# Kernel optimization log

Hardware: AMD Instinct MI355X
Metric: run time of the kernel (lower is better)

Reference implementation:

```python
import jax, jax.numpy as jnp
import numpy as np

B, S, D, H = 2, 2048, 1024, 16
MASK_VAL = -50000.0

def setup_inputs() -> dict:
    key = jax.random.key(0)
    k1, k2, k3, k4 = jax.random.split(key, 4)
    # weights stored as [in, out] so projection is x @ W (equals torch Linear with W.T)
    s = 1.0 / np.sqrt(D)
    return {
        "x": jax.random.normal(k1, (B, S, D), dtype=jnp.float32),
        "Wq": jax.random.normal(k2, (D, D), dtype=jnp.float32) * s,
        "Wkv": jax.random.normal(k3, (D, 2 * D), dtype=jnp.float32) * s,
        "Wo": jax.random.normal(k4, (D, D), dtype=jnp.float32) * s,
    }

def reference(x, Wq, Wkv, Wo):
    b, sl, d = x.shape
    h = H
    hd = d // h
    scale = hd ** (-0.5)
    q = x @ Wq                      # [b, sl, d]
    kv = x @ Wkv                    # [b, sl, 2d]
    k, v = jnp.split(kv, 2, axis=-1)
    # [b, h, s, hd]
    q = q.reshape(b, sl, h, hd).transpose(0, 2, 1, 3)
    k = k.reshape(b, sl, h, hd).transpose(0, 2, 1, 3)
    v = v.reshape(b, sl, h, hd).transpose(0, 2, 1, 3)
    dots = jnp.einsum('bhid,bhjd->bhij', q * scale, k)  # [b,h,s,s]
    # causal: strictly-upper-triangular entries set to MASK_VAL
    causal = jnp.tril(jnp.ones((sl, sl), dtype=bool))
    dots = jnp.where(causal, dots, MASK_VAL)
    attn = jax.nn.softmax(dots, axis=-1)
    out = jnp.einsum('bhij,bhjd->bihd', attn, v).reshape(b, sl, d)
    return out @ Wo
```

## Files before the change

kernel.cpp:

```cpp
#include <hip/hip_runtime.h>

typedef __bf16 bf16_t;
typedef unsigned short u16;
typedef __attribute__((ext_vector_type(8))) __bf16 bf16x8;
typedef __attribute__((ext_vector_type(4))) float f32x4;
typedef __attribute__((ext_vector_type(4))) u16 u16x4;
typedef __attribute__((ext_vector_type(8))) u16 u16x8;

#define SS 2048
#define PSTR 72

__device__ __forceinline__ u16 f2b(float f) {
    return __builtin_bit_cast(u16, (__bf16)f);
}

__device__ __forceinline__ float fexp2(float x) {
#if __has_builtin(__builtin_amdgcn_exp2f)
    return __builtin_amdgcn_exp2f(x);
#else
    float r;
    asm("v_exp_f32 %0, %1" : "=v"(r) : "v"(x));
    return r;
#endif
}

__device__ __forceinline__ void async_copy16(const u16* g, u16* l) {
    __builtin_amdgcn_global_load_lds(
        (__attribute__((address_space(1))) void*)(u16*)g,
        (__attribute__((address_space(3))) void*)l, 16, 0, 0);
}

__device__ __forceinline__ bf16x8 ldfrag(const u16* p) {
    return __builtin_bit_cast(bf16x8, *(const u16x8*)p);
}

__global__ __launch_bounds__(256)
void cast_x_kernel(const float* __restrict__ x, u16* __restrict__ xb) {
    size_t i = ((size_t)blockIdx.x * 256 + threadIdx.x) * 8;
    float4 a = *(const float4*)(x + i);
    float4 b = *(const float4*)(x + i + 4);
    u16x8 o;
    o[0] = f2b(a.x); o[1] = f2b(a.y); o[2] = f2b(a.z); o[3] = f2b(a.w);
    o[4] = f2b(b.x); o[5] = f2b(b.y); o[6] = f2b(b.z); o[7] = f2b(b.w);
    *(u16x8*)(xb + i) = o;
}

__global__ __launch_bounds__(256)
void transpose_all(const float* __restrict__ Wq, const float* __restrict__ Wkv,
                   const float* __restrict__ Wo, u16* __restrict__ WcatT,
                   u16* __restrict__ WoT) {
    const int z = blockIdx.z;
    if (z != 1 && blockIdx.y >= 16) return;
    const float* src; u16* dst; int N; float scale;
    if (z == 0)      { src = Wq;  dst = WcatT;               N = 1024; scale = 0.125f * 1.44269504089f; }
    else if (z == 1) { src = Wkv; dst = WcatT + 1024 * 1024; N = 2048; scale = 1.0f; }
    else             { src = Wo;  dst = WoT;                 N = 1024; scale = 1.0f; }
    __shared__ __attribute__((aligned(16))) u16 tile[64][72];
    const int k0 = blockIdx.x * 64, n0 = blockIdx.y * 64;
    const int tid = threadIdx.x;
#pragma unroll
    for (int p = 0; p < 4; ++p) {
        int c = p * 256 + tid;
        int r = c >> 4, c4 = c & 15;
        float4 v = *(const float4*)(src + (size_t)(k0 + r) * N + n0 + c4 * 4);
        u16x4 o;
        o[0] = f2b(v.x * scale); o[1] = f2b(v.y * scale);
        o[2] = f2b(v.z * scale); o[3] = f2b(v.w * scale);
        *(u16x4*)&tile[r][c4 * 4] = o;
    }
    __syncthreads();
#pragma unroll
    for (int p = 0; p < 4; ++p) {
        int c = p * 256 + tid;
        int n = c >> 4, k4 = c & 15;
        u16x4 o;
#pragma unroll
        for (int i = 0; i < 4; ++i) o[i] = tile[k4 * 4 + i][n];
        *(u16x4*)(dst + (size_t)(n0 + n) * 1024 + k0 + k4 * 4) = o;
    }
}

__global__ __launch_bounds__(256)
void transpose_v(const u16* __restrict__ QKV, u16* __restrict__ VTg) {
    __shared__ __attribute__((aligned(16))) u16 tile[64][72];
    const int s0 = blockIdx.x * 64;
    const int bh = blockIdx.y;
    const int b = bh >> 4, h = bh & 15;
    const int tid = threadIdx.x;
    const u16* src = QKV + ((size_t)b * SS + s0) * 3072 + 2048 + h * 64;
#pragma unroll
    for (int p = 0; p < 4; ++p) {
        int c = p * 256 + tid;
        int s = c >> 4, h4 = c & 15;
        *(u16x4*)&tile[s][h4 * 4] = *(const u16x4*)(src + (size_t)s * 3072 + h4 * 4);
    }
    __syncthreads();
    u16* dst = VTg + (size_t)bh * 64 * 2048 + s0;
#pragma unroll
    for (int p = 0; p < 4; ++p) {
        int c = p * 256 + tid;
        int hd = c >> 4, s4 = c & 15;
        u16x4 o;
#pragma unroll
        for (int i = 0; i < 4; ++i) o[i] = tile[s4 * 4 + i][hd];
        *(u16x4*)(dst + (size_t)hd * 2048 + s4 * 4) = o;
    }
}

template <typename OutT>
__global__ __launch_bounds__(256, 2)
void gemm_bt(const u16* __restrict__ A, const u16* __restrict__ BT,
             OutT* __restrict__ C, int M, int N, int K) {
    __shared__ __attribute__((aligned(16))) u16 As[128 * 32];
    __shared__ __attribute__((aligned(16))) u16 Bs[128 * 32];
    const int tid = threadIdx.x;
    const int wave = tid >> 6, lane = tid & 63;
    const int l15 = lane & 15, quad = lane >> 4;
    const int m0 = blockIdx.y * 128, n0 = blockIdx.x * 128;
    const int wm = (wave >> 1) * 64, wn = (wave & 1) * 64;
    const f32x4 zero = {0.f, 0.f, 0.f, 0.f};
    f32x4 acc[4][4];
#pragma unroll
    for (int i = 0; i < 4; ++i)
#pragma unroll
        for (int j = 0; j < 4; ++j) acc[i][j] = zero;
    const int r0 = tid >> 2, kc = (tid & 3) * 8;
    for (int k0 = 0; k0 < K; k0 += 32) {
        async_copy16(A + (size_t)(m0 + r0) * K + k0 + kc, As + tid * 8);
        async_copy16(BT + (size_t)(n0 + r0) * K + k0 + kc, Bs + tid * 8);
        async_copy16(A + (size_t)(m0 + 64 + r0) * K + k0 + kc, As + (256 + tid) * 8);
        async_copy16(BT + (size_t)(n0 + 64 + r0) * K + k0 + kc, Bs + (256 + tid) * 8);
        __syncthreads();
        bf16x8 af[4], bf[4];
#pragma unroll
        for (int t = 0; t < 4; ++t) {
            af[t] = ldfrag(As + (wm + t * 16 + l15) * 32 + quad * 8);
            bf[t] = ldfrag(Bs + (wn + t * 16 + l15) * 32 + quad * 8);
        }
#pragma unroll
        for (int mt = 0; mt < 4; ++mt)
#pragma unroll
            for (int nt = 0; nt < 4; ++nt)
                acc[mt][nt] = __builtin_amdgcn_mfma_f32_16x16x32_bf16(
                    af[mt], bf[nt], acc[mt][nt], 0, 0, 0);
        __syncthreads();
    }
#pragma unroll
    for (int mt = 0; mt < 4; ++mt)
#pragma unroll
        for (int nt = 0; nt < 4; ++nt) {
            const int n = n0 + wn + nt * 16 + l15;
#pragma unroll
            for (int r = 0; r < 4; ++r) {
                const int m = m0 + wm + mt * 16 + quad * 4 + r;
                float v = acc[mt][nt][r];
                if constexpr (sizeof(OutT) == 2) C[(size_t)m * N + n] = (OutT)f2b(v);
                else                             C[(size_t)m * N + n] = v;
            }
        }
}

__global__ __launch_bounds__(256, 2)
void gemm_bt64(const u16* __restrict__ A, const u16* __restrict__ BT,
               float* __restrict__ C, int M, int N, int K) {
    __shared__ __attribute__((aligned(16))) u16 As[128 * 32];
    __shared__ __attribute__((aligned(16))) u16 Bs[64 * 32];
    const int tid = threadIdx.x;
    const int wave = tid >> 6, lane = tid & 63;
    const int l15 = lane & 15, quad = lane >> 4;
    const int m0 = blockIdx.y * 128, n0 = blockIdx.x * 64;
    const int wm = (wave >> 1) * 64, wn = (wave & 1) * 32;
    const f32x4 zero = {0.f, 0.f, 0.f, 0.f};
    f32x4 acc[4][2];
#pragma unroll
    for (int i = 0; i < 4; ++i)
#pragma unroll
        for (int j = 0; j < 2; ++j) acc[i][j] = zero;
    const int r0 = tid >> 2, kc = (tid & 3) * 8;
    for (int k0 = 0; k0 < K; k0 += 32) {
        async_copy16(A + (size_t)(m0 + r0) * K + k0 + kc, As + tid * 8);
        async_copy16(A + (size_t)(m0 + 64 + r0) * K + k0 + kc, As + (256 + tid) * 8);
        async_copy16(BT + (size_t)(n0 + r0) * K + k0 + kc, Bs + tid * 8);
        __syncthreads();
        bf16x8 af[4], bf[2];
#pragma unroll
        for (int t = 0; t < 4; ++t)
            af[t] = ldfrag(As + (wm + t * 16 + l15) * 32 + quad * 8);
#pragma unroll
        for (int t = 0; t < 2; ++t)
            bf[t] = ldfrag(Bs + (wn + t * 16 + l15) * 32 + quad * 8);
#pragma unroll
        for (int mt = 0; mt < 4; ++mt)
#pragma unroll
            for (int nt = 0; nt < 2; ++nt)
                acc[mt][nt] = __builtin_amdgcn_mfma_f32_16x16x32_bf16(
                    af[mt], bf[nt], acc[mt][nt], 0, 0, 0);
        __syncthreads();
    }
#pragma unroll
    for (int mt = 0; mt < 4; ++mt)
#pragma unroll
        for (int nt = 0; nt < 2; ++nt) {
            const int n = n0 + wn + nt * 16 + l15;
#pragma unroll
            for (int r = 0; r < 4; ++r) {
                const int m = m0 + wm + mt * 16 + quad * 4 + r;
                C[(size_t)m * N + n] = acc[mt][nt][r];
            }
        }
}

__device__ __forceinline__ void attn_scoreT(
    const bf16x8 (&kf)[2], const bf16x8 (&qf)[4][2],
    float (&l_i)[4], u16* __restrict__ P, bool diag, int w16, int l15, int quad) {
    const f32x4 cinit = {-10.f, -10.f, -10.f, -10.f};
#pragma unroll
    for (int t = 0; t < 4; ++t) {
        f32x4 a = __builtin_amdgcn_mfma_f32_16x16x32_bf16(kf[0], qf[t][0], cinit, 0, 0, 0);
        f32x4 s = __builtin_amdgcn_mfma_f32_16x16x32_bf16(kf[1], qf[t][1], a, 0, 0, 0);
        if (diag) {
#pragma unroll
            for (int r = 0; r < 4; ++r)
                if (w16 + quad * 4 + r > t * 16 + l15) s[r] = -1e30f;
        }
        u16x4 pk;
        float acc = 0.f;
#pragma unroll
        for (int r = 0; r < 4; ++r) {
            float pv = fexp2(s[r]);
            acc += pv;
            pk[r] = f2b(pv);
        }
        l_i[t] += acc;
        *(u16x4*)(P + (t * 16 + l15) * PSTR + w16 + quad * 4) = pk;
    }
}

__device__ __forceinline__ void attn_pv(
    const u16* __restrict__ P, const bf16x8 (&vf)[4][2],
    f32x4 (&O)[4], int l15, int quad) {
    bf16x8 pf0 = ldfrag(P + l15 * PSTR + quad * 8);
    bf16x8 pf1 = ldfrag(P + l15 * PSTR + 32 + quad * 8);
#pragma unroll
    for (int nt = 0; nt < 4; ++nt) {
        O[nt] = __builtin_amdgcn_mfma_f32_16x16x32_bf16(pf0, vf[nt][0], O[nt], 0, 0, 0);
        O[nt] = __builtin_amdgcn_mfma_f32_16x16x32_bf16(pf1, vf[nt][1], O[nt], 0, 0, 0);
    }
}

__global__ __launch_bounds__(256, 2)
void attn_kernel(const u16* __restrict__ QKV, const u16* __restrict__ VTg,
                 u16* __restrict__ AO) {
    __shared__ __attribute__((aligned(16))) u16 Kt[2][2 * 64 * 32];
    __shared__ __attribute__((aligned(16))) u16 Vt[2][2 * 64 * 32];
    __shared__ __attribute__((aligned(16))) u16 Pq[128 * PSTR];
    const int tid = threadIdx.x;
    const int wave = tid >> 6, lane = tid & 63;
    const int l15 = lane & 15, quad = lane >> 4;
    const int w16 = wave * 16;
    const int bh = blockIdx.y, b = bh >> 4, h = bh & 15;
    const int xe = b ? 15 - (int)blockIdx.x : (int)blockIdx.x;
    const int qbA = 31 - xe, qbB = xe;
    const int qA0 = qbA * 64, qB0 = qbB * 64;
    const size_t bS = (size_t)b * SS;
    const u16* vbase = VTg + (size_t)bh * 64 * 2048;
    const int rr = (tid >> 2) & 63, kc8 = (tid & 3) * 8;

    {
        const u16* qsrcA = QKV + (bS + qA0 + rr) * 3072 + h * 64 + kc8;
        async_copy16(qsrcA,      Pq + tid * 8);
        async_copy16(qsrcA + 32, Pq + (256 + tid) * 8);
        const u16* qsrcB = QKV + (bS + qB0 + rr) * 3072 + h * 64 + kc8;
        async_copy16(qsrcB,      Pq + (512 + tid) * 8);
        async_copy16(qsrcB + 32, Pq + (768 + tid) * 8);
        const u16* ksrc = QKV + (bS + rr) * 3072 + 1024 + h * 64 + kc8;
        async_copy16(ksrc,      Kt[0] + tid * 8);
        async_copy16(ksrc + 32, Kt[0] + (256 + tid) * 8);
        const u16* vsrc = vbase + (size_t)rr * 2048 + kc8;
        async_copy16(vsrc,      Vt[0] + tid * 8);
        async_copy16(vsrc + 32, Vt[0] + (256 + tid) * 8);
    }
    __syncthreads();
    bf16x8 qfA[4][2], qfB[4][2];
#pragma unroll
    for (int t = 0; t < 4; ++t)
#pragma unroll
        for (int ks = 0; ks < 2; ++ks) {
            qfA[t][ks] = ldfrag(Pq + ks * 2048 + (t * 16 + l15) * 32 + quad * 8);
            qfB[t][ks] = ldfrag(Pq + 4096 + ks * 2048 + (t * 16 + l15) * 32 + quad * 8);
        }
    __syncthreads();

    u16* PA = Pq;
    u16* PB = Pq + 64 * PSTR;
    float lA[4], lB[4];
    f32x4 OA[4], OB[4];
    const f32x4 zero = {0.f, 0.f, 0.f, 0.f};
#pragma unroll
    for (int t = 0; t < 4; ++t) { lA[t] = lB[t] = 0.f; }
#pragma unroll
    for (int nt = 0; nt < 4; ++nt) { OA[nt] = zero; OB[nt] = zero; }

    for (int j = 0; j <= qbA; ++j) {
        if (j < qbA) {
            const int kv1 = (j + 1) * 64;
            const int nb = (j + 1) & 1;
            const u16* ksrc = QKV + (bS + kv1 + rr) * 3072 + 1024 + h * 64 + kc8;
            async_copy16(ksrc,      Kt[nb] + tid * 8);
            async_copy16(ksrc + 32, Kt[nb] + (256 + tid) * 8);
            const u16* vsrc = vbase + (size_t)rr * 2048 + kv1 + kc8;
            async_copy16(vsrc,      Vt[nb] + tid * 8);
            async_copy16(vsrc + 32, Vt[nb] + (256 + tid) * 8);
        }
        const bool bAct = (j <= qbB);
        const u16* KB = Kt[j & 1];
        const u16* VB = Vt[j & 1];
        bf16x8 kf[2];
#pragma unroll
        for (int ks = 0; ks < 2; ++ks)
            kf[ks] = ldfrag(KB + ks * 2048 + (w16 + l15) * 32 + quad * 8);
        attn_scoreT(kf, qfA, lA, PA, j == qbA, w16, l15, quad);
        if (bAct)
            attn_scoreT(kf, qfB, lB, PB, j == qbB, w16, l15, quad);
        __syncthreads();
        bf16x8 vf[4][2];
#pragma unroll
        for (int nt = 0; nt < 4; ++nt)
#pragma unroll
            for (int ks = 0; ks < 2; ++ks)
                vf[nt][ks] = ldfrag(VB + ks * 2048 + (nt * 16 + l15) * 32 + quad * 8);
        attn_pv(PA + w16 * PSTR, vf, OA, l15, quad);
        if (bAct)
            attn_pv(PB + w16 * PSTR, vf, OB, l15, quad);
        __syncthreads();
    }

    float* lsh = (float*)Kt;
#pragma unroll
    for (int t = 0; t < 4; ++t) {
        float sA = lA[t];
        sA += __shfl_xor(sA, 16); sA += __shfl_xor(sA, 32);
        float sB = lB[t];
        sB += __shfl_xor(sB, 16); sB += __shfl_xor(sB, 32);
        if (lane < 16) {
            lsh[(t * 16 + l15) * 4 + wave] = sA;
            lsh[(64 + t * 16 + l15) * 4 + wave] = sB;
        }
    }
    __syncthreads();
#pragma unroll
    for (int r = 0; r < 4; ++r) {
        const int qlA = w16 + quad * 4 + r;
        f32x4 la = *(const f32x4*)&lsh[qlA * 4];
        f32x4 lb = *(const f32x4*)&lsh[(64 + qlA) * 4];
        float invA = 1.0f / (la[0] + la[1] + la[2] + la[3]);
        float invB = 1.0f / (lb[0] + lb[1] + lb[2] + lb[3]);
        size_t rowA = bS + (size_t)qA0 + qlA;
        size_t rowB = bS + (size_t)qB0 + qlA;
#pragma unroll
        for (int nt = 0; nt < 4; ++nt) {
            AO[rowA * 1024 + h * 64 + nt * 16 + l15] = f2b(OA[nt][r] * invA);
            AO[rowB * 1024 + h * 64 + nt * 16 + l15] = f2b(OB[nt][r] * invB);
        }
    }
}

extern "C" void kernel_launch(void* const* d_in, const int* in_sizes, int n_in,
                              void* d_out, int out_size, void* d_ws, size_t ws_size,
                              hipStream_t stream) {
    (void)in_sizes; (void)n_in; (void)out_size; (void)ws_size;
    const float* x   = (const float*)d_in[0];
    const float* Wq  = (const float*)d_in[1];
    const float* Wkv = (const float*)d_in[2];
    const float* Wo  = (const float*)d_in[3];
    float* out = (float*)d_out;
    char* ws = (char*)d_ws;
    u16* xb    = (u16*)(ws);
    u16* WcatT = (u16*)(ws + (size_t)(8 << 20));
    u16* WoT   = (u16*)(ws + (size_t)(14 << 20));
    u16* QKV   = (u16*)(ws + (size_t)(16 << 20));
    u16* VTb   = (u16*)(ws + (size_t)(40 << 20));
    u16* AO    = xb;

    cast_x_kernel<<<2048, 256, 0, stream>>>(x, xb);
    transpose_all<<<dim3(16, 32, 3), 256, 0, stream>>>(Wq, Wkv, Wo, WcatT, WoT);
    gemm_bt<u16><<<dim3(24, 32), 256, 0, stream>>>(xb, WcatT, QKV, 4096, 3072, 1024);
    transpose_v<<<dim3(32, 32), 256, 0, stream>>>(QKV, VTb);
    attn_kernel<<<dim3(16, 32), 256, 0, stream>>>(QKV, VTb, AO);
    gemm_bt64<<<dim3(16, 32), 256, 0, stream>>>(AO, WoT, out, 4096, 1024, 1024);
}
```

Baseline: 183.5 us.

## Load K and V fragments directly from global into registers, drop LDS staging

Removes the shared-memory double buffers for K and V tiles and instead has each wave load its K fragment (software-prefetched one iteration ahead into a register double buffer) and all V fragments directly from global memory. The intent is to cut LDS traffic, async-copy overhead and LDS footprint, which could allow more occupancy. In exchange, every wave redundantly fetches the full V tile from global/L2 each iteration, V loads are no longer prefetched ahead, and the reduction scratch moves onto the P buffer.

```diff
diff --git a/kernel.cpp b/kernel.cpp
--- a/kernel.cpp
+++ b/kernel.cpp
@@ -251,8 +251,6 @@
 __global__ __launch_bounds__(256, 2)
 void attn_kernel(const u16* __restrict__ QKV, const u16* __restrict__ VTg,
                  u16* __restrict__ AO) {
-    __shared__ __attribute__((aligned(16))) u16 Kt[2][2 * 64 * 32];
-    __shared__ __attribute__((aligned(16))) u16 Vt[2][2 * 64 * 32];
     __shared__ __attribute__((aligned(16))) u16 Pq[128 * PSTR];
     const int tid = threadIdx.x;
     const int wave = tid >> 6, lane = tid & 63;
@@ -264,6 +262,7 @@
     const int qA0 = qbA * 64, qB0 = qbB * 64;
     const size_t bS = (size_t)b * SS;
     const u16* vbase = VTg + (size_t)bh * 64 * 2048;
+    const u16* kbase = QKV + bS * 3072 + 1024 + h * 64;
     const int rr = (tid >> 2) & 63, kc8 = (tid & 3) * 8;
 
     {
@@ -273,12 +272,6 @@
         const u16* qsrcB = QKV + (bS + qB0 + rr) * 3072 + h * 64 + kc8;
         async_copy16(qsrcB,      Pq + (512 + tid) * 8);
         async_copy16(qsrcB + 32, Pq + (768 + tid) * 8);
-        const u16* ksrc = QKV + (bS + rr) * 3072 + 1024 + h * 64 + kc8;
-        async_copy16(ksrc,      Kt[0] + tid * 8);
-        async_copy16(ksrc + 32, Kt[0] + (256 + tid) * 8);
-        const u16* vsrc = vbase + (size_t)rr * 2048 + kc8;
-        async_copy16(vsrc,      Vt[0] + tid * 8);
-        async_copy16(vsrc + 32, Vt[0] + (256 + tid) * 8);
     }
     __syncthreads();
     bf16x8 qfA[4][2], qfB[4][2];
@@ -301,41 +294,42 @@
 #pragma unroll
     for (int nt = 0; nt < 4; ++nt) { OA[nt] = zero; OB[nt] = zero; }
 
+    bf16x8 kf[2][2];
+    {
+        const u16* kp = kbase + (size_t)(w16 + l15) * 3072 + quad * 8;
+        kf[0][0] = ldfrag(kp);
+        kf[0][1] = ldfrag(kp + 32);
+    }
+
     for (int j = 0; j <= qbA; ++j) {
+        const int kv0 = j * 64;
+        bf16x8 vf[4][2];
+        {
+            const u16* vp = vbase + (size_t)l15 * 2048 + kv0 + quad * 8;
+#pragma unroll
+            for (int nt = 0; nt < 4; ++nt)
+#pragma unroll
+                for (int ks = 0; ks < 2; ++ks)
+                    vf[nt][ks] = ldfrag(vp + (size_t)nt * 16 * 2048 + ks * 32);
+        }
+        const bool bAct = (j <= qbB);
+        const int cb = j & 1;
+        attn_scoreT(kf[cb], qfA, lA, PA, j == qbA, w16, l15, quad);
+        if (bAct)
+            attn_scoreT(kf[cb], qfB, lB, PB, j == qbB, w16, l15, quad);
         if (j < qbA) {
-            const int kv1 = (j + 1) * 64;
-            const int nb = (j + 1) & 1;
-            const u16* ksrc = QKV + (bS + kv1 + rr) * 3072 + 1024 + h * 64 + kc8;
-            async_copy16(ksrc,      Kt[nb] + tid * 8);
-            async_copy16(ksrc + 32, Kt[nb] + (256 + tid) * 8);
-            const u16* vsrc = vbase + (size_t)rr * 2048 + kv1 + kc8;
-            async_copy16(vsrc,      Vt[nb] + tid * 8);
-            async_copy16(vsrc + 32, Vt[nb] + (256 + tid) * 8);
-        }
-        const bool bAct = (j <= qbB);
-        const u16* KB = Kt[j & 1];
-        const u16* VB = Vt[j & 1];
-        bf16x8 kf[2];
-#pragma unroll
-        for (int ks = 0; ks < 2; ++ks)
-            kf[ks] = ldfrag(KB + ks * 2048 + (w16 + l15) * 32 + quad * 8);
-        attn_scoreT(kf, qfA, lA, PA, j == qbA, w16, l15, quad);
-        if (bAct)
-            attn_scoreT(kf, qfB, lB, PB, j == qbB, w16, l15, quad);
-        __syncthreads();
-        bf16x8 vf[4][2];
-#pragma unroll
-        for (int nt = 0; nt < 4; ++nt)
-#pragma unroll
-            for (int ks = 0; ks < 2; ++ks)
-                vf[nt][ks] = ldfrag(VB + ks * 2048 + (nt * 16 + l15) * 32 + quad * 8);
+            const u16* kp = kbase + (size_t)(kv0 + 64 + w16 + l15) * 3072 + quad * 8;
+            kf[cb ^ 1][0] = ldfrag(kp);
+            kf[cb ^ 1][1] = ldfrag(kp + 32);
+        }
+        __syncthreads();
         attn_pv(PA + w16 * PSTR, vf, OA, l15, quad);
         if (bAct)
             attn_pv(PB + w16 * PSTR, vf, OB, l15, quad);
         __syncthreads();
     }
 
-    float* lsh = (float*)Kt;
+    float* lsh = (float*)Pq;
 #pragma unroll
     for (int t = 0; t < 4; ++t) {
         float sA = lA[t];
```

After: 495.3 us. 170% more time.
